# Kernel tuning notes

Measured on AMD Instinct MI355X. Metric: run time of the kernel, lower is better.

## Reference

```python
import jax, jax.numpy as jnp
import numpy as np


def setup_inputs() -> dict:
    key = jax.random.key(0)
    k1, k2, k3 = jax.random.split(key, 3)
    N, RANK, M = 1024, 16, 4096
    W = jax.random.normal(k1, (N, RANK), dtype=jnp.float32)
    H = jax.random.normal(k2, (RANK, M), dtype=jnp.float32)
    tau_tilde = jax.random.uniform(k3, (N, RANK), dtype=jnp.float32)
    return {"W": W, "H": H, "tau_tilde": tau_tilde}


def reference(W, H, tau_tilde):
    # W: (N, rank), H: (rank, M), tau_tilde: (N, rank)
    M = H.shape[1]
    Nf = M // 2 + 1
    # FFT of softplus(H), keep non-negative freqs, rebuild full spectrum by conjugate symmetry
    Hf = jnp.fft.fft(jax.nn.softplus(H), axis=1)[:, :Nf]            # (rank, Nf) complex
    Hf_reverse = Hf[:, 1:Nf - 1][:, ::-1]                            # flip of interior bins
    Hft = jnp.concatenate([Hf, jnp.conj(Hf_reverse)], axis=1)        # (rank, M)
    f = jnp.arange(M, dtype=jnp.float32) / M                         # (M,)
    # omega[N,d,M] = exp(-i 2 pi tau[N,d] f[M]); Wf = softplus(W)[...,None] * omega
    omega = jnp.exp(-2j * jnp.pi * (tau_tilde[:, :, None] * f[None, None, :]))
    Wf = jax.nn.softplus(W)[:, :, None].astype(omega.dtype) * omega  # (N, rank, M)
    V = jnp.einsum('NdM,dM->NM', Wf, Hft)                            # (N, M) complex
    return V
```

## Files before the change

kernel.cpp:

```cpp
#include <hip/hip_runtime.h>
#include <math.h>

#define MLEN 4096
#define RANK 16
#define NROWS 1024
#define LNB 8

__device__ float2 g_Hft[RANK * MLEN];

__device__ __forceinline__ float softplus_f(float x) {
    return fmaxf(x, 0.0f) + log1pf(__expf(-fabsf(x)));
}

__global__ __launch_bounds__(1024) void fft_rows_kernel(const float* __restrict__ H) {
    __shared__ float2 buf[MLEN];
    const int row = blockIdx.x;
    const int t   = threadIdx.x;
    const float* h = H + row * MLEN;

    for (int i = t; i < MLEN; i += 1024) {
        int j = (int)(__brev((unsigned)i) >> 20);
        buf[j] = make_float2(softplus_f(h[i]), 0.0f);
    }
    __syncthreads();

    #pragma unroll
    for (int s = 0; s < 12; s += 2) {
        const int h1 = 1 << s;
        const int p  = t & (h1 - 1);
        const int k  = ((t >> s) << (s + 2)) + p;
        const float rA = (float)p * (1.0f / (float)(h1 << 2));
        const float ca = __builtin_amdgcn_cosf(rA);
        const float sa = __builtin_amdgcn_sinf(rA);
        const float c1 = ca * ca - sa * sa;
        const float s1 = 2.0f * ca * sa;

        const float2 a0 = buf[k];
        const float2 a1 = buf[k + h1];
        const float2 a2 = buf[k + 2 * h1];
        const float2 a3 = buf[k + 3 * h1];

        const float2 w1a1 = make_float2(c1 * a1.x + s1 * a1.y, c1 * a1.y - s1 * a1.x);
        const float2 w1a3 = make_float2(c1 * a3.x + s1 * a3.y, c1 * a3.y - s1 * a3.x);
        const float2 u0 = make_float2(a0.x + w1a1.x, a0.y + w1a1.y);
        const float2 u1 = make_float2(a0.x - w1a1.x, a0.y - w1a1.y);
        const float2 u2 = make_float2(a2.x + w1a3.x, a2.y + w1a3.y);
        const float2 u3 = make_float2(a2.x - w1a3.x, a2.y - w1a3.y);

        const float2 wAu2 = make_float2(ca * u2.x + sa * u2.y, ca * u2.y - sa * u2.x);
        const float2 v    = make_float2(ca * u3.x + sa * u3.y, ca * u3.y - sa * u3.x);
        const float2 wBu3 = make_float2(v.y, -v.x);

        buf[k]          = make_float2(u0.x + wAu2.x, u0.y + wAu2.y);
        buf[k + h1]     = make_float2(u1.x + wBu3.x, u1.y + wBu3.y);
        buf[k + 2 * h1] = make_float2(u0.x - wAu2.x, u0.y - wAu2.y);
        buf[k + 3 * h1] = make_float2(u1.x - wBu3.x, u1.y - wBu3.y);
        __syncthreads();
    }

    for (int i = t; i < MLEN; i += 1024) {
        g_Hft[row * MLEN + i] = buf[i];
    }
}

__global__ __launch_bounds__(256) void mix_mirror_kernel(const float* __restrict__ W,
                                                         const float* __restrict__ tau,
                                                         float* __restrict__ out) {
    __shared__ __align__(16) float sw_s[LNB * RANK];
    __shared__ __align__(16) float tv_s[LNB * RANK];
    __shared__ __align__(16) float qc_s[LNB * RANK];
    __shared__ __align__(16) float qi_s[LNB * RANK];

    const int tid = threadIdx.x;
    const int n0  = blockIdx.y * LNB;

    if (tid < LNB * RANK) {
        const float sw = softplus_f(W[n0 * RANK + tid]);
        const float tv = tau[n0 * RANK + tid];
        const float c2 = __builtin_amdgcn_cosf(tv);
        const float s2 = __builtin_amdgcn_sinf(tv);
        sw_s[tid] = sw;
        tv_s[tid] = tv;
        qc_s[tid] = sw * c2;
        qi_s[tid] = -sw * s2;
    }
    __syncthreads();

    const int a  = blockIdx.x * 256 + tid + 1;
    const int mm = MLEN - a;
    const float fa = (float)a * (1.0f / (float)MLEN);

    float2 h[RANK];
    #pragma unroll
    for (int d = 0; d < RANK; ++d) h[d] = g_Hft[d * MLEN + a];

    #pragma unroll 1
    for (int ln = 0; ln < LNB; ++ln) {
        const int base = ln * RANK;
        float ar = 0.0f, aw = 0.0f;
        #pragma unroll
        for (int d = 0; d < RANK; ++d) {
            const float tv = tv_s[base + d];
            const float sw = sw_s[base + d];
            const float qc = qc_s[base + d];
            const float qi = qi_s[base + d];
            const float r  = tv * fa;
            const float c  = __builtin_amdgcn_cosf(r);
            const float s  = __builtin_amdgcn_sinf(r);
            const float tre = fmaf(s, h[d].y, c * h[d].x);
            const float tim = fmaf(c, h[d].y, -s * h[d].x);
            ar = fmaf(sw, tre, ar);
            aw = fmaf(qc, tre, fmaf(qi, tim, aw));
        }
        const int rowbase = (n0 + ln) * MLEN;
        out[rowbase + a]  = ar;
        out[rowbase + mm] = aw;
    }

    if (blockIdx.x == 0 && tid == 0) {
        float h0[RANK];
        #pragma unroll
        for (int d = 0; d < RANK; ++d) h0[d] = g_Hft[d * MLEN].x;
        for (int ln = 0; ln < LNB; ++ln) {
            float v = 0.0f;
            #pragma unroll
            for (int d = 0; d < RANK; ++d) v = fmaf(sw_s[ln * RANK + d], h0[d], v);
            out[(n0 + ln) * MLEN] = v;
        }
    }
}

__global__ __launch_bounds__(256) void mix_generic_kernel(const float* __restrict__ W,
                                                          const float* __restrict__ tau,
                                                          float* __restrict__ out,
                                                          int out_size_floats) {
    __shared__ float sw_s[256];
    __shared__ float tau_s[256];
    const int tid = threadIdx.x;
    const int m   = blockIdx.x * 256 + tid;
    const int n0  = blockIdx.y * 16;
    sw_s[tid]  = softplus_f(W[n0 * RANK + tid]);
    tau_s[tid] = tau[n0 * RANK + tid];
    __syncthreads();
    float2 h[RANK];
    #pragma unroll
    for (int d = 0; d < RANK; ++d) h[d] = g_Hft[d * MLEN + m];
    const float fm = (float)m * (1.0f / (float)MLEN);
    #pragma unroll 1
    for (int ln = 0; ln < 16; ++ln) {
        float ar = 0.0f, ai = 0.0f;
        #pragma unroll
        for (int d = 0; d < RANK; ++d) {
            const float r = tau_s[ln * RANK + d] * fm;
            const float c = __builtin_amdgcn_cosf(r);
            const float s = __builtin_amdgcn_sinf(r);
            const float sw = sw_s[ln * RANK + d];
            ar = fmaf(sw, fmaf(s, h[d].y, c * h[d].x), ar);
            ai = fmaf(sw, fmaf(c, h[d].y, -s * h[d].x), ai);
        }
        const long long fi = 2LL * ((long long)(n0 + ln) * MLEN + m);
        if (fi + 1 < (long long)out_size_floats) {
            out[fi]     = ar;
            out[fi + 1] = ai;
        }
    }
}

extern "C" void kernel_launch(void* const* d_in, const int* in_sizes, int n_in,
                              void* d_out, int out_size, void* d_ws, size_t ws_size,
                              hipStream_t stream) {
    const float* W   = (const float*)d_in[0];
    const float* H   = (const float*)d_in[1];
    const float* tau = (const float*)d_in[2];
    float* out = (float*)d_out;
    (void)d_ws; (void)ws_size; (void)in_sizes; (void)n_in;

    fft_rows_kernel<<<dim3(RANK), dim3(1024), 0, stream>>>(H);

    if (out_size == NROWS * MLEN) {
        mix_mirror_kernel<<<dim3(8, NROWS / LNB), dim3(256), 0, stream>>>(W, tau, out);
    } else {
        mix_generic_kernel<<<dim3(MLEN / 256, NROWS / 16), dim3(256), 0, stream>>>(
            W, tau, out, out_size);
    }
}
```

Before: 82.19 us.

## Pad FFT shared buffer, fuse first radix-4 stage, pack mix params into float4

The FFT kernel pads its shared buffer (one extra slot every 16 entries) to reduce LDS bank conflicts. It also folds the bit-reversal load and the first radix-4 stage into registers, which drops one barrier stage. The mix kernel packs its four per-(row, rank) parameters into a single float4 shared array so each iteration does one wide LDS load, and it halves rows per block (LNB 8 to 4) while adding an occupancy hint. Smaller row blocks double the grid and the reloads of the H spectrum into registers, in exchange for more parallelism.

```diff
diff --git a/kernel.cpp b/kernel.cpp
--- a/kernel.cpp
+++ b/kernel.cpp
@@ -4,7 +4,7 @@
 #define MLEN 4096
 #define RANK 16
 #define NROWS 1024
-#define LNB 8
+#define LNB 4
 
 __device__ float2 g_Hft[RANK * MLEN];
 
@@ -12,20 +12,30 @@
     return fmaxf(x, 0.0f) + log1pf(__expf(-fabsf(x)));
 }
 
+#define MAP(i) ((i) + ((i) >> 4))
+
 __global__ __launch_bounds__(1024) void fft_rows_kernel(const float* __restrict__ H) {
-    __shared__ float2 buf[MLEN];
+    __shared__ float2 buf[MLEN + MLEN / 16];
     const int row = blockIdx.x;
     const int t   = threadIdx.x;
     const float* h = H + row * MLEN;
 
-    for (int i = t; i < MLEN; i += 1024) {
-        int j = (int)(__brev((unsigned)i) >> 20);
-        buf[j] = make_float2(softplus_f(h[i]), 0.0f);
-    }
+    const int r10 = (int)(__brev((unsigned)t) >> 22);
+    const float a0 = softplus_f(h[r10]);
+    const float a1 = softplus_f(h[r10 + 2048]);
+    const float a2 = softplus_f(h[r10 + 1024]);
+    const float a3 = softplus_f(h[r10 + 3072]);
+    const float u0 = a0 + a1, u1 = a0 - a1;
+    const float u2 = a2 + a3, u3 = a2 - a3;
+    const int k0 = t << 2;
+    buf[MAP(k0)]     = make_float2(u0 + u2, 0.0f);
+    buf[MAP(k0 + 1)] = make_float2(u1, -u3);
+    buf[MAP(k0 + 2)] = make_float2(u0 - u2, 0.0f);
+    buf[MAP(k0 + 3)] = make_float2(u1, u3);
     __syncthreads();
 
     #pragma unroll
-    for (int s = 0; s < 12; s += 2) {
+    for (int s = 2; s < 12; s += 2) {
         const int h1 = 1 << s;
         const int p  = t & (h1 - 1);
         const int k  = ((t >> s) << (s + 2)) + p;
@@ -35,41 +45,38 @@
         const float c1 = ca * ca - sa * sa;
         const float s1 = 2.0f * ca * sa;
 
-        const float2 a0 = buf[k];
-        const float2 a1 = buf[k + h1];
-        const float2 a2 = buf[k + 2 * h1];
-        const float2 a3 = buf[k + 3 * h1];
+        const float2 a0c = buf[MAP(k)];
+        const float2 a1c = buf[MAP(k + h1)];
+        const float2 a2c = buf[MAP(k + 2 * h1)];
+        const float2 a3c = buf[MAP(k + 3 * h1)];
 
-        const float2 w1a1 = make_float2(c1 * a1.x + s1 * a1.y, c1 * a1.y - s1 * a1.x);
-        const float2 w1a3 = make_float2(c1 * a3.x + s1 * a3.y, c1 * a3.y - s1 * a3.x);
-        const float2 u0 = make_float2(a0.x + w1a1.x, a0.y + w1a1.y);
-        const float2 u1 = make_float2(a0.x - w1a1.x, a0.y - w1a1.y);
-        const float2 u2 = make_float2(a2.x + w1a3.x, a2.y + w1a3.y);
-        const float2 u3 = make_float2(a2.x - w1a3.x, a2.y - w1a3.y);
+        const float2 w1a1 = make_float2(c1 * a1c.x + s1 * a1c.y, c1 * a1c.y - s1 * a1c.x);
+        const float2 w1a3 = make_float2(c1 * a3c.x + s1 * a3c.y, c1 * a3c.y - s1 * a3c.x);
+        const float2 v0 = make_float2(a0c.x + w1a1.x, a0c.y + w1a1.y);
+        const float2 v1 = make_float2(a0c.x - w1a1.x, a0c.y - w1a1.y);
+        const float2 v2 = make_float2(a2c.x + w1a3.x, a2c.y + w1a3.y);
+        const float2 v3 = make_float2(a2c.x - w1a3.x, a2c.y - w1a3.y);
 
-        const float2 wAu2 = make_float2(ca * u2.x + sa * u2.y, ca * u2.y - sa * u2.x);
-        const float2 v    = make_float2(ca * u3.x + sa * u3.y, ca * u3.y - sa * u3.x);
-        const float2 wBu3 = make_float2(v.y, -v.x);
+        const float2 wAv2 = make_float2(ca * v2.x + sa * v2.y, ca * v2.y - sa * v2.x);
+        const float2 w    = make_float2(ca * v3.x + sa * v3.y, ca * v3.y - sa * v3.x);
+        const float2 wBv3 = make_float2(w.y, -w.x);
 
-        buf[k]          = make_float2(u0.x + wAu2.x, u0.y + wAu2.y);
-        buf[k + h1]     = make_float2(u1.x + wBu3.x, u1.y + wBu3.y);
-        buf[k + 2 * h1] = make_float2(u0.x - wAu2.x, u0.y - wAu2.y);
-        buf[k + 3 * h1] = make_float2(u1.x - wBu3.x, u1.y - wBu3.y);
+        buf[MAP(k)]          = make_float2(v0.x + wAv2.x, v0.y + wAv2.y);
+        buf[MAP(k + h1)]     = make_float2(v1.x + wBv3.x, v1.y + wBv3.y);
+        buf[MAP(k + 2 * h1)] = make_float2(v0.x - wAv2.x, v0.y - wAv2.y);
+        buf[MAP(k + 3 * h1)] = make_float2(v1.x - wBv3.x, v1.y - wBv3.y);
         __syncthreads();
     }
 
     for (int i = t; i < MLEN; i += 1024) {
-        g_Hft[row * MLEN + i] = buf[i];
+        g_Hft[row * MLEN + i] = buf[MAP(i)];
     }
 }
 
-__global__ __launch_bounds__(256) void mix_mirror_kernel(const float* __restrict__ W,
-                                                         const float* __restrict__ tau,
-                                                         float* __restrict__ out) {
-    __shared__ __align__(16) float sw_s[LNB * RANK];
-    __shared__ __align__(16) float tv_s[LNB * RANK];
-    __shared__ __align__(16) float qc_s[LNB * RANK];
-    __shared__ __align__(16) float qi_s[LNB * RANK];
+__global__ __launch_bounds__(256, 6) void mix_mirror_kernel(const float* __restrict__ W,
+                                                            const float* __restrict__ tau,
+                                                            float* __restrict__ out) {
+    __shared__ __align__(16) float4 prm[LNB * RANK];
 
     const int tid = threadIdx.x;
     const int n0  = blockIdx.y * LNB;
@@ -79,10 +86,7 @@
         const float tv = tau[n0 * RANK + tid];
         const float c2 = __builtin_amdgcn_cosf(tv);
         const float s2 = __builtin_amdgcn_sinf(tv);
-        sw_s[tid] = sw;
-        tv_s[tid] = tv;
-        qc_s[tid] = sw * c2;
-        qi_s[tid] = -sw * s2;
+        prm[tid] = make_float4(sw, tv, sw * c2, -sw * s2);
     }
     __syncthreads();
 
@@ -96,21 +100,17 @@
 
     #pragma unroll 1
     for (int ln = 0; ln < LNB; ++ln) {
-        const int base = ln * RANK;
         float ar = 0.0f, aw = 0.0f;
         #pragma unroll
         for (int d = 0; d < RANK; ++d) {
-            const float tv = tv_s[base + d];
-            const float sw = sw_s[base + d];
-            const float qc = qc_s[base + d];
-            const float qi = qi_s[base + d];
-            const float r  = tv * fa;
+            const float4 P = prm[ln * RANK + d];
+            const float r  = P.y * fa;
             const float c  = __builtin_amdgcn_cosf(r);
             const float s  = __builtin_amdgcn_sinf(r);
             const float tre = fmaf(s, h[d].y, c * h[d].x);
             const float tim = fmaf(c, h[d].y, -s * h[d].x);
-            ar = fmaf(sw, tre, ar);
-            aw = fmaf(qc, tre, fmaf(qi, tim, aw));
+            ar = fmaf(P.x, tre, ar);
+            aw = fmaf(P.z, tre, fmaf(P.w, tim, aw));
         }
         const int rowbase = (n0 + ln) * MLEN;
         out[rowbase + a]  = ar;
@@ -124,7 +124,7 @@
         for (int ln = 0; ln < LNB; ++ln) {
             float v = 0.0f;
             #pragma unroll
-            for (int d = 0; d < RANK; ++d) v = fmaf(sw_s[ln * RANK + d], h0[d], v);
+            for (int d = 0; d < RANK; ++d) v = fmaf(prm[ln * RANK + d].x, h0[d], v);
             out[(n0 + ln) * MLEN] = v;
         }
     }
```

After: 81.29 us. About the same (-1.1%).
